# Kernel optimization log

Measured on AMD Instinct MI355X. Metric: run time of the kernel, lower is better.

Reference implementation:

```python
import jax, jax.numpy as jnp
import numpy as np

N_NODES = 50000
N_EDGES = 800000
IN_FEATS = 256
OUT_FEATS = 64


def setup_inputs() -> dict:
    key = jax.random.key(0)
    k1, k2, k3, k4 = jax.random.split(key, 4)
    feat = jax.random.normal(k1, (N_NODES, IN_FEATS), dtype=jnp.float32)
    # xavier_uniform-like init for weight
    limit = float(np.sqrt(6.0 / (IN_FEATS + OUT_FEATS)))
    weight = jax.random.uniform(k2, (IN_FEATS, OUT_FEATS), dtype=jnp.float32,
                                minval=-limit, maxval=limit)
    bias = jnp.zeros((OUT_FEATS,), dtype=jnp.float32)
    src = jax.random.randint(k3, (N_EDGES,), 0, N_NODES, dtype=jnp.int32)
    dst = jax.random.randint(k4, (N_EDGES,), 0, N_NODES, dtype=jnp.int32)
    return {"feat": feat, "weight": weight, "bias": bias, "src": src, "dst": dst}


def reference(feat, weight, bias, src, dst):
    # GCN GraphConv with norm='both', edge_weight=None, activation=None.
    n = feat.shape[0]
    ones_e = jnp.ones(src.shape[0], dtype=feat.dtype)
    out_deg = jnp.clip(jax.ops.segment_sum(ones_e, src, num_segments=n), 1.0)
    in_deg = jnp.clip(jax.ops.segment_sum(ones_e, dst, num_segments=n), 1.0)

    # left/both pre-normalization by out-degree^{-1/2}
    feat_src = feat * (out_deg ** -0.5)[:, None]

    # lin_before_mp: in_feats (256) > out_feats (64) -> project first
    h = feat_src @ weight  # [N, out_feats]

    # copy_u + sum aggregation: gather from src, scatter-add to dst
    rst = jax.ops.segment_sum(h[src], dst, num_segments=n)  # [N, out_feats]

    # right/both post-normalization by in-degree^{-1/2}, then bias
    rst = rst * (in_deg ** -0.5)[:, None] + bias
    return rst
```

## Files before the change

kernel.cpp:

```cpp
#include <hip/hip_runtime.h>
#include <hip/hip_bf16.h>

#define N_NODES 50000
#define N_EDGES 800000
#define IN_F 256
#define OUT_F 64
#define NBUCKET 196
#define HCOPIES 32
#define EDGES_PER_COPY 25000
#define HWORDS 25000
#define PBLOCKS 200
#define EDGES_PER_PBLOCK 4000
#define MAXB 6144

__global__ __launch_bounds__(1024)
void hist_kernel(const int* __restrict__ src, const int* __restrict__ dst,
                 unsigned* __restrict__ scratch) {
    __shared__ unsigned lh[HWORDS];
    int tid = threadIdx.x, b = blockIdx.x;
    const int* idx = (b < HCOPIES) ? src : dst;
    int k = b & 31;
    int e0 = k * EDGES_PER_COPY;
    for (int i = tid; i < HWORDS; i += 1024) lh[i] = 0;
    __syncthreads();
    for (int i = tid; i < EDGES_PER_COPY; i += 1024) {
        int id = idx[e0 + i];
        atomicAdd(&lh[id >> 1], (id & 1) ? 0x10000u : 1u);
    }
    __syncthreads();
    unsigned* outp = scratch + (size_t)b * HWORDS;
    for (int i = tid; i < HWORDS; i += 1024) outp[i] = lh[i];
}

__global__ void reduce_kernel(const unsigned* __restrict__ scratch,
                              int* __restrict__ cnt_out, int* __restrict__ cnt_in) {
    int t = blockIdx.x * blockDim.x + threadIdx.x;
    if (t >= 2 * HWORDS) return;
    int side = (t >= HWORDS);
    int j = side ? t - HWORDS : t;
    const unsigned* base = scratch + (size_t)(side ? HCOPIES : 0) * HWORDS + j;
    unsigned lo = 0, hi = 0;
    for (int k = 0; k < HCOPIES; ++k) {
        unsigned v = base[(size_t)k * HWORDS];
        lo += v & 0xFFFFu; hi += v >> 16;
    }
    int* dstp = side ? cnt_in : cnt_out;
    dstp[2 * j] = (int)lo;
    dstp[2 * j + 1] = (int)hi;
}

__global__ void scan_kernel(const int* __restrict__ cnt_in,
                            int* __restrict__ bucket_off, int* __restrict__ bucket_cursor) {
    __shared__ int tot[256];
    int t = threadIdx.x;
    int s = 0;
    if (t < NBUCKET) {
        int base = t * 256;
        int lim = min(256, N_NODES - base);
        for (int i = 0; i < lim; ++i) s += cnt_in[base + i];
    }
    tot[t] = s;
    __syncthreads();
    for (int off = 1; off < 256; off <<= 1) {
        int v = (t >= off) ? tot[t - off] : 0;
        __syncthreads();
        tot[t] += v;
        __syncthreads();
    }
    if (t < NBUCKET) {
        int excl = tot[t] - s;
        bucket_off[t] = excl;
        bucket_cursor[t * 16] = excl;
    }
    if (t == NBUCKET - 1) bucket_off[NBUCKET] = tot[t];
}

__global__ __launch_bounds__(1024)
void partition_kernel(const int* __restrict__ src, const int* __restrict__ dst,
                      int* __restrict__ bucket_cursor, unsigned* __restrict__ recs) {
    __shared__ int lcnt[NBUCKET], lbase[NBUCKET];
    int tid = threadIdx.x;
    int e0 = blockIdx.x * EDGES_PER_PBLOCK;
    if (tid < NBUCKET) lcnt[tid] = 0;
    __syncthreads();
    unsigned rec[4]; int bkt[4], rnk[4];
#pragma unroll
    for (int j = 0; j < 4; ++j) {
        int i = j * 1024 + tid;
        bkt[j] = -1;
        if (i < EDGES_PER_PBLOCK) {
            int e = e0 + i;
            int s = src[e], d = dst[e];
            bkt[j] = d >> 8;
            rec[j] = (unsigned)s | ((unsigned)(d & 255) << 16);
            rnk[j] = atomicAdd(&lcnt[bkt[j]], 1);
        }
    }
    __syncthreads();
    if (tid < NBUCKET) lbase[tid] = atomicAdd(&bucket_cursor[tid * 16], lcnt[tid]);
    __syncthreads();
#pragma unroll
    for (int j = 0; j < 4; ++j)
        if (bkt[j] >= 0) recs[lbase[bkt[j]] + rnk[j]] = rec[j];
}

__global__ __launch_bounds__(256)
void gemm_kernel(const float* __restrict__ feat, const float* __restrict__ weight,
                 const int* __restrict__ cnt_out, __hip_bfloat16* __restrict__ h) {
    __shared__ __align__(16) float As[64 * 64];
    __shared__ __align__(16) float Ws[64 * 64];
    int tid = threadIdx.x;
    int block_row = blockIdx.x * 64;
    int cg = tid & 31;
    int rg = tid >> 5;
    float acc[8][2] = {};

    for (int kt = 0; kt < 4; ++kt) {
#pragma unroll
        for (int j = 0; j < 4; ++j) {
            int ldi = j * 256 + tid;
            int row = ldi >> 4;
            int c4  = ldi & 15;
            int grow = block_row + row;
            int grc = (grow < N_NODES) ? grow : (N_NODES - 1);
            float4 a = *(const float4*)&feat[grc * IN_F + kt * 64 + c4 * 4];
            float sc = rsqrtf((float)max(cnt_out[grc], 1));
            a.x *= sc; a.y *= sc; a.z *= sc; a.w *= sc;
            *(float4*)&As[row * 64 + c4 * 4] = a;
            float4 wv = *(const float4*)&weight[(kt * 64 + row) * OUT_F + c4 * 4];
            *(float4*)&Ws[row * 64 + c4 * 4] = wv;
        }
        __syncthreads();
#pragma unroll
        for (int kk4 = 0; kk4 < 16; ++kk4) {
            float4 a[8];
#pragma unroll
            for (int i = 0; i < 8; ++i)
                a[i] = *(const float4*)&As[(rg * 8 + i) * 64 + kk4 * 4];
#pragma unroll
            for (int j = 0; j < 4; ++j) {
                float w0 = Ws[(kk4 * 4 + j) * 64 + cg];
                float w1 = Ws[(kk4 * 4 + j) * 64 + cg + 32];
#pragma unroll
                for (int i = 0; i < 8; ++i) {
                    float av = (&a[i].x)[j];
                    acc[i][0] = fmaf(av, w0, acc[i][0]);
                    acc[i][1] = fmaf(av, w1, acc[i][1]);
                }
            }
        }
        __syncthreads();
    }
#pragma unroll
    for (int i = 0; i < 8; ++i) {
        int row = block_row + rg * 8 + i;
        if (row < N_NODES) {
            h[row * OUT_F + cg]      = __float2bfloat16(acc[i][0]);
            h[row * OUT_F + cg + 32] = __float2bfloat16(acc[i][1]);
        }
    }
}

__global__ __launch_bounds__(1024)
void aggregate_kernel(const __hip_bfloat16* __restrict__ h, const unsigned* __restrict__ recs,
                      const int* __restrict__ bucket_off,
                      const float* __restrict__ bias, float* __restrict__ out) {
    __shared__ int cnt[256], off[256], cur[256];
    __shared__ unsigned short order[MAXB];
    int tid = threadIdx.x, lane = tid & 63, w = tid >> 6;
    int b = blockIdx.x;
    if (tid < 256) { cnt[tid] = 0; cur[tid] = 0; }
    __syncthreads();
    int start = bucket_off[b], end = bucket_off[b + 1];
    int n = end - start;

    for (int i = tid; i < n; i += 1024)
        atomicAdd(&cnt[(recs[start + i] >> 16) & 255u], 1);
    __syncthreads();

    if (tid < 256) off[tid] = cnt[tid];
    __syncthreads();
    for (int o = 1; o < 256; o <<= 1) {
        int y = (tid < 256 && tid >= o) ? off[tid - o] : 0;
        __syncthreads();
        if (tid < 256) off[tid] += y;
        __syncthreads();
    }

    for (int i = tid; i < n; i += 1024) {
        unsigned rec = recs[start + i];
        int dl = (rec >> 16) & 255u;
        int r = atomicAdd(&cur[dl], 1);
        int pos = off[dl] - cnt[dl] + r;
        if (pos < MAXB) order[pos] = (unsigned short)(rec & 0xFFFFu);
    }
    __syncthreads();

    float bv = bias[lane];
    int gbase = b * 256;
    for (int nd = w; nd < 256; nd += 16) {
        int g = gbase + nd;
        if (g >= N_NODES) continue;
        int m = cnt[nd];
        int s0 = off[nd] - m;
        float acc = 0.f;
        int k = 0;
        for (; k + 4 <= m; k += 4) {
            int a0 = order[s0 + k], a1 = order[s0 + k + 1];
            int a2 = order[s0 + k + 2], a3 = order[s0 + k + 3];
            acc += __bfloat162float(h[a0 * OUT_F + lane]) + __bfloat162float(h[a1 * OUT_F + lane])
                 + __bfloat162float(h[a2 * OUT_F + lane]) + __bfloat162float(h[a3 * OUT_F + lane]);
        }
        for (; k < m; ++k) acc += __bfloat162float(h[order[s0 + k] * OUT_F + lane]);
        float sc = rsqrtf((float)max(m, 1));
        out[g * OUT_F + lane] = fmaf(acc, sc, bv);
    }
}

extern "C" void kernel_launch(void* const* d_in, const int* in_sizes, int n_in,
                              void* d_out, int out_size, void* d_ws, size_t ws_size,
                              hipStream_t stream) {
    const float* feat   = (const float*)d_in[0];
    const float* weight = (const float*)d_in[1];
    const float* bias   = (const float*)d_in[2];
    const int*   src    = (const int*)d_in[3];
    const int*   dst    = (const int*)d_in[4];
    float* out = (float*)d_out;

    int* ws            = (int*)d_ws;
    int* cnt_out       = ws;
    int* cnt_in        = ws + 50000;
    int* bucket_off    = ws + 100000;
    int* bucket_cursor = ws + 100224;
    unsigned* scratch  = (unsigned*)(ws + 103424);
    unsigned* recs     = (unsigned*)(ws + 1703424);
    __hip_bfloat16* h  = (__hip_bfloat16*)(ws + 2503424);

    hist_kernel<<<2 * HCOPIES, 1024, 0, stream>>>(src, dst, scratch);
    reduce_kernel<<<(2 * HWORDS + 1023) / 1024, 1024, 0, stream>>>(scratch, cnt_out, cnt_in);
    scan_kernel<<<1, 256, 0, stream>>>(cnt_in, bucket_off, bucket_cursor);
    partition_kernel<<<PBLOCKS, 1024, 0, stream>>>(src, dst, bucket_cursor, recs);
    gemm_kernel<<<(N_NODES + 63) / 64, 256, 0, stream>>>(feat, weight, cnt_out, h);
    aggregate_kernel<<<NBUCKET, 1024, 0, stream>>>(h, recs, bucket_off, bias, out);
}
```

Baseline: 198.2 us.

## Rewrite projection GEMM with bf16 MFMA and swizzled transposed weight tile

Replaces the FP32 FMA shared-memory GEMM with MFMA 16x16x32 bf16 instructions. Each block converts the full weight matrix to bf16, stores it transposed in LDS with an XOR swizzle, and loads A fragments straight from global memory with the degree scaling and bf16 conversion applied in registers. This cuts the ALU cost and the A-tile staging, but adds bf16 rounding of both operands and a per-block reload and conversion of the whole weight matrix.

```diff
diff --git a/kernel.cpp b/kernel.cpp
--- a/kernel.cpp
+++ b/kernel.cpp
@@ -13,6 +13,9 @@
 #define EDGES_PER_PBLOCK 4000
 #define MAXB 6144
 
+using bf16x8 = __attribute__((ext_vector_type(8))) short;
+using f32x4  = __attribute__((ext_vector_type(4))) float;
+
 __global__ __launch_bounds__(1024)
 void hist_kernel(const int* __restrict__ src, const int* __restrict__ dst,
                  unsigned* __restrict__ scratch) {
@@ -107,56 +110,65 @@
 __global__ __launch_bounds__(256)
 void gemm_kernel(const float* __restrict__ feat, const float* __restrict__ weight,
                  const int* __restrict__ cnt_out, __hip_bfloat16* __restrict__ h) {
-    __shared__ __align__(16) float As[64 * 64];
-    __shared__ __align__(16) float Ws[64 * 64];
+    __shared__ __align__(16) short Wt[64 * 256];
     int tid = threadIdx.x;
-    int block_row = blockIdx.x * 64;
-    int cg = tid & 31;
-    int rg = tid >> 5;
-    float acc[8][2] = {};
-
-    for (int kt = 0; kt < 4; ++kt) {
+
+#pragma unroll
+    for (int it = 0; it < 16; ++it) {
+        int idx = it * 256 + tid;
+        int k  = idx >> 4;
+        int n4 = (idx & 15) * 4;
+        float4 wv = *(const float4*)&weight[k * OUT_F + n4];
 #pragma unroll
         for (int j = 0; j < 4; ++j) {
-            int ldi = j * 256 + tid;
-            int row = ldi >> 4;
-            int c4  = ldi & 15;
-            int grow = block_row + row;
-            int grc = (grow < N_NODES) ? grow : (N_NODES - 1);
-            float4 a = *(const float4*)&feat[grc * IN_F + kt * 64 + c4 * 4];
-            float sc = rsqrtf((float)max(cnt_out[grc], 1));
-            a.x *= sc; a.y *= sc; a.z *= sc; a.w *= sc;
-            *(float4*)&As[row * 64 + c4 * 4] = a;
-            float4 wv = *(const float4*)&weight[(kt * 64 + row) * OUT_F + c4 * 4];
-            *(float4*)&Ws[row * 64 + c4 * 4] = wv;
-        }
-        __syncthreads();
-#pragma unroll
-        for (int kk4 = 0; kk4 < 16; ++kk4) {
-            float4 a[8];
-#pragma unroll
-            for (int i = 0; i < 8; ++i)
-                a[i] = *(const float4*)&As[(rg * 8 + i) * 64 + kk4 * 4];
-#pragma unroll
-            for (int j = 0; j < 4; ++j) {
-                float w0 = Ws[(kk4 * 4 + j) * 64 + cg];
-                float w1 = Ws[(kk4 * 4 + j) * 64 + cg + 32];
-#pragma unroll
-                for (int i = 0; i < 8; ++i) {
-                    float av = (&a[i].x)[j];
-                    acc[i][0] = fmaf(av, w0, acc[i][0]);
-                    acc[i][1] = fmaf(av, w1, acc[i][1]);
-                }
-            }
-        }
-        __syncthreads();
-    }
-#pragma unroll
-    for (int i = 0; i < 8; ++i) {
-        int row = block_row + rg * 8 + i;
-        if (row < N_NODES) {
-            h[row * OUT_F + cg]      = __float2bfloat16(acc[i][0]);
-            h[row * OUT_F + cg + 32] = __float2bfloat16(acc[i][1]);
+            int n = n4 + j;
+            __hip_bfloat16 bv = __float2bfloat16((&wv.x)[j]);
+            int byte = (n * 512 + k * 2) ^ ((n & 7) << 4);
+            *(short*)((char*)Wt + byte) = *(short*)&bv;
+        }
+    }
+
+    int lane = tid & 63, w = tid >> 6;
+    int rowbase = blockIdx.x * 64 + w * 16;
+    int arow = rowbase + (lane & 15);
+    int arc = min(arow, N_NODES - 1);
+    float sc = rsqrtf((float)max(cnt_out[arc], 1));
+    const float* ap = &feat[arc * IN_F + (lane >> 4) * 8];
+    __syncthreads();
+
+    f32x4 acc[4];
+#pragma unroll
+    for (int c = 0; c < 4; ++c) acc[c] = (f32x4){0.f, 0.f, 0.f, 0.f};
+
+#pragma unroll
+    for (int ks = 0; ks < 8; ++ks) {
+        float4 a0 = *(const float4*)(ap + ks * 32);
+        float4 a1 = *(const float4*)(ap + ks * 32 + 4);
+        bf16x8 af;
+#pragma unroll
+        for (int j = 0; j < 4; ++j) {
+            __hip_bfloat16 b0 = __float2bfloat16((&a0.x)[j] * sc);
+            __hip_bfloat16 b1 = __float2bfloat16((&a1.x)[j] * sc);
+            af[j]     = *(short*)&b0;
+            af[j + 4] = *(short*)&b1;
+        }
+        int kb = ks * 64 + (lane >> 4) * 16;
+#pragma unroll
+        for (int c = 0; c < 4; ++c) {
+            int n = c * 16 + (lane & 15);
+            int byte = (n * 512 + kb) ^ ((n & 7) << 4);
+            bf16x8 bfv = *(const bf16x8*)((const char*)Wt + byte);
+            acc[c] = __builtin_amdgcn_mfma_f32_16x16x32_bf16(af, bfv, acc[c], 0, 0, 0);
+        }
+    }
+
+#pragma unroll
+    for (int c = 0; c < 4; ++c) {
+#pragma unroll
+        for (int r = 0; r < 4; ++r) {
+            int row = rowbase + (lane >> 4) * 4 + r;
+            if (row < N_NODES)
+                h[row * OUT_F + c * 16 + (lane & 15)] = __float2bfloat16(acc[c][r]);
         }
     }
 }
```

Measured after the change: 179.5 us. -9.5%, faster.
